# Optimization experiments

Hardware: AMD Instinct MI355X
Metric: run time of the kernel (lower is better)

## Reference

```python
import jax, jax.numpy as jnp
import numpy as np

WINDOW_SIZE = 128
NEG = -1e9

def setup_inputs() -> dict:
    key = jax.random.key(0)
    kq, kk, kv = jax.random.split(key, 3)
    B, H, T, D = 2, 16, 2048, 64
    q = jax.random.normal(kq, (B, H, T, D), dtype=jnp.float32)
    k = jax.random.normal(kk, (B, H, T, D), dtype=jnp.float32)
    v = jax.random.normal(kv, (B, H, T, D), dtype=jnp.float32)
    return {"q": q, "k": k, "v": v}

def reference(q, k, v):
    # q,k,v: (B, H, T, D)
    D = q.shape[-1]
    Tq, Tk = q.shape[2], k.shape[2]
    scale = 1.0 / jnp.sqrt(jnp.asarray(D, dtype=q.dtype))
    scores = jnp.einsum('bhqd,bhkd->bhqk', q, k) * scale  # (B,H,Tq,Tk)
    dist = jnp.abs(jnp.arange(Tq)[:, None] - jnp.arange(Tk)[None, :])
    window_mask = dist <= WINDOW_SIZE  # (Tq,Tk)
    scores = jnp.where(window_mask[None, None], scores, jnp.asarray(NEG, dtype=scores.dtype))
    attn = jax.nn.softmax(scores, axis=-1)
    output = jnp.einsum('bhqk,bhkd->bhqd', attn, v)
    return (output, attn)
```

## Files before the change

kernel.cpp:

```cpp
#include <hip/hip_runtime.h>
#include <hip/hip_bf16.h>

typedef short bf16x8 __attribute__((ext_vector_type(8)));
typedef short bf16x4 __attribute__((ext_vector_type(4)));
typedef float f32x4 __attribute__((ext_vector_type(4)));

#define T_DIM 2048
#define D_DIM 64
#define WIN 128
#define QBLK 64
#define ACCT 17
#define NEGBIG -1e30f

__device__ __forceinline__ short f2b(float x) {
  __hip_bfloat16 h = __float2bfloat16(x);
  return *reinterpret_cast<short*>(&h);
}
__device__ __forceinline__ float b2f(short s) {
  unsigned u = ((unsigned)(unsigned short)s) << 16;
  return __builtin_bit_cast(float, u);
}
__device__ __forceinline__ bf16x8 cvt8(f32x4 a, f32x4 b) {
  bf16x8 r;
  r[0] = f2b(a[0]); r[1] = f2b(a[1]); r[2] = f2b(a[2]); r[3] = f2b(a[3]);
  r[4] = f2b(b[0]); r[5] = f2b(b[1]); r[6] = f2b(b[2]); r[7] = f2b(b[3]);
  return r;
}
__device__ __forceinline__ int swz(int row, int b) { return row * 640 + (b ^ ((row & 7) << 4)); }

__global__ __launch_bounds__(256, 2) void lsa_one(
    const float* __restrict__ Qg, const float* __restrict__ Kg,
    const float* __restrict__ Vg, float* __restrict__ Og,
    float* __restrict__ Ag) {
  const int tid = threadIdx.x;
  const int work = ((blockIdx.x & 7) << 7) + (blockIdx.x >> 3);
  const int bh = work >> 5;
  const int q0 = (work & 31) * QBLK;
  int kstart = q0 - WIN; if (kstart < 0) kstart = 0;
  int kend = q0 + QBLK + WIN; if (kend > T_DIM) kend = T_DIM;
  const int KW = kend - kstart;
  const int nkt = KW >> 4;

  const float* qptr = Qg + (size_t)bh * (T_DIM * D_DIM);
  const float* kptr = Kg + (size_t)bh * (T_DIM * D_DIM);
  const float* vptr = Vg + (size_t)bh * (T_DIM * D_DIM);
  float* optr = Og + (size_t)bh * (T_DIM * D_DIM);
  float* aptr = Ag + (size_t)bh * ((size_t)T_DIM * T_DIM);

  __shared__ __align__(16) char Vb[D_DIM * 640];
  __shared__ __align__(16) char Pb[QBLK * 640];

  for (int idx = tid; idx < KW * 16; idx += 256) {
    const int r = idx >> 4, c4 = idx & 15;
    f32x4 f = *(const f32x4*)(vptr + (size_t)(kstart + r) * D_DIM + c4 * 4);
    const int d0 = c4 * 4;
    *(short*)(Vb + swz(d0 + 0, r * 2)) = f2b(f[0]);
    *(short*)(Vb + swz(d0 + 1, r * 2)) = f2b(f[1]);
    *(short*)(Vb + swz(d0 + 2, r * 2)) = f2b(f[2]);
    *(short*)(Vb + swz(d0 + 3, r * 2)) = f2b(f[3]);
  }

  const int lane = tid & 63, w = tid >> 6, c = lane & 15, hi = lane >> 4;

  const float* qrow = qptr + (size_t)(q0 + w * 16 + c) * D_DIM + 8 * hi;
  const bf16x8 qb0 = cvt8(*(const f32x4*)qrow, *(const f32x4*)(qrow + 4));
  const bf16x8 qb1 = cvt8(*(const f32x4*)(qrow + 32), *(const f32x4*)(qrow + 36));

  int klo = q0 + w * 16 - WIN - kstart; if (klo < 0) klo = 0;
  const int kt0 = klo >> 4;
  int kt1 = (q0 + w * 16 + 15 + WIN + 1 - kstart + 15) >> 4; if (kt1 > nkt) kt1 = nkt;
  const int s0 = kt0 >> 1, s1 = (kt1 + 1) >> 1;
  const int nlive = kt1 - kt0;

  f32x4 acc[ACCT];
#pragma unroll
  for (int i = 0; i < ACCT; ++i) {
    acc[i] = (f32x4){0.f, 0.f, 0.f, 0.f};
    if (i < nlive) {
      const float* kr = kptr + (size_t)(kstart + (kt0 + i) * 16 + c) * D_DIM + 8 * hi;
      const bf16x8 b0 = cvt8(*(const f32x4*)kr, *(const f32x4*)(kr + 4));
      const bf16x8 b1 = cvt8(*(const f32x4*)(kr + 32), *(const f32x4*)(kr + 36));
      acc[i] = __builtin_amdgcn_mfma_f32_16x16x32_bf16(b0, qb0, acc[i], 0, 0, 0);
      acc[i] = __builtin_amdgcn_mfma_f32_16x16x32_bf16(b1, qb1, acc[i], 0, 0, 0);
    }
  }

  const int qr = q0 + w * 16 + c;
  const int kb = kstart + 4 * hi;
  float m = NEGBIG;
#pragma unroll
  for (int i = 0; i < ACCT; ++i)
    if (i < nlive) {
#pragma unroll
      for (int j = 0; j < 4; ++j) {
        float s = acc[i][j] * 0.125f;
        const int kcol = kb + (kt0 + i) * 16 + j;
        int dist = qr - kcol; dist = dist < 0 ? -dist : dist;
        s = (dist <= WIN) ? s : NEGBIG;
        acc[i][j] = s;
        m = fmaxf(m, s);
      }
    }
  m = fmaxf(m, __shfl_xor(m, 16));
  m = fmaxf(m, __shfl_xor(m, 32));
  float sum = 0.f;
#pragma unroll
  for (int i = 0; i < ACCT; ++i)
    if (i < nlive) {
#pragma unroll
      for (int j = 0; j < 4; ++j) {
        const float p = __expf(acc[i][j] - m);
        acc[i][j] = p;
        sum += p;
      }
    }
  sum += __shfl_xor(sum, 16);
  sum += __shfl_xor(sum, 32);
  const float inv = 1.f / sum;

  const int prow = w * 16 + c;
#pragma unroll
  for (int i = 0; i < ACCT; ++i)
    if (i < nlive) {
      bf16x4 pk;
#pragma unroll
      for (int j = 0; j < 4; ++j) pk[j] = f2b(acc[i][j] * inv);
      *(bf16x4*)(Pb + swz(prow, 32 * (kt0 + i) + 8 * hi)) = pk;
    }
  {
    const bf16x4 z4 = {0, 0, 0, 0};
    for (int t = 0; t < kt0; ++t) *(bf16x4*)(Pb + swz(prow, 32 * t + 8 * hi)) = z4;
    for (int t = kt1; t < nkt; ++t) *(bf16x4*)(Pb + swz(prow, 32 * t + 8 * hi)) = z4;
  }

  for (int rr = 0; rr < 16; ++rr) {
    const int r = w * 16 + rr;
    float* dst = aptr + (size_t)(q0 + r) * T_DIM;
#pragma unroll
    for (int i = 0; i < 8; ++i) {
      const int col = i * 256 + lane * 4;
      f32x4 val = {0.f, 0.f, 0.f, 0.f};
      if (col >= kstart && col < kend) {
        const bf16x4 pv = *(const bf16x4*)(Pb + swz(r, (col - kstart) * 2));
        val[0] = b2f(pv[0]); val[1] = b2f(pv[1]); val[2] = b2f(pv[2]); val[3] = b2f(pv[3]);
      }
      __builtin_nontemporal_store(val, (f32x4*)(dst + col));
    }
  }

  __syncthreads();

  f32x4 ov[4];
#pragma unroll
  for (int dt = 0; dt < 4; ++dt) ov[dt] = (f32x4){0.f, 0.f, 0.f, 0.f};
  for (int s = s0; s < s1; ++s) {
    const bf16x8 pa = *(const bf16x8*)(Pb + swz(w * 16 + c, 64 * s + 16 * hi));
#pragma unroll
    for (int dt = 0; dt < 4; ++dt) {
      const bf16x8 vb = *(const bf16x8*)(Vb + swz(dt * 16 + c, 64 * s + 16 * hi));
      ov[dt] = __builtin_amdgcn_mfma_f32_16x16x32_bf16(pa, vb, ov[dt], 0, 0, 0);
    }
  }
#pragma unroll
  for (int dt = 0; dt < 4; ++dt)
#pragma unroll
    for (int j = 0; j < 4; ++j)
      __builtin_nontemporal_store(
          ov[dt][j], optr + (size_t)(q0 + w * 16 + 4 * hi + j) * D_DIM + dt * 16 + c);
}

extern "C" void kernel_launch(void* const* d_in, const int* in_sizes, int n_in,
                              void* d_out, int out_size, void* d_ws, size_t ws_size,
                              hipStream_t stream) {
  const float* q = (const float*)d_in[0];
  const float* k = (const float*)d_in[1];
  const float* v = (const float*)d_in[2];
  float* out = (float*)d_out;
  float* attn = out + (size_t)2 * 16 * T_DIM * D_DIM;
  lsa_one<<<dim3(2 * 16 * (T_DIM / QBLK)), dim3(256), 0, stream>>>(q, k, v, out, attn);
}
```

Before: 129.0 us.

## Pre-convert Q/K/V to bf16 in workspace and split into multi-kernel pipeline

Adds pre-pass kernels that convert Q and K to bf16 and write V transposed as bf16 into the workspace. The main kernel then reads bf16 operands directly, fetching V fragments from global memory instead of staging them in shared memory, which allows a third resident block per CU. It also writes the output tile before the attention-matrix stores. This removes the redundant per-block fp32-to-bf16 conversion of overlapping K and V windows, at the cost of three extra launches and an extra pass over the inputs. The original kernel remains as a fallback when the workspace is too small.

```diff
diff --git a/kernel.cpp b/kernel.cpp
--- a/kernel.cpp
+++ b/kernel.cpp
@@ -7,6 +7,8 @@
 
 #define T_DIM 2048
 #define D_DIM 64
+#define BH 32
+#define NELEM (BH * T_DIM * D_DIM)
 #define WIN 128
 #define QBLK 64
 #define ACCT 17
@@ -28,7 +30,171 @@
 }
 __device__ __forceinline__ int swz(int row, int b) { return row * 640 + (b ^ ((row & 7) << 4)); }
 
-__global__ __launch_bounds__(256, 2) void lsa_one(
+__global__ __launch_bounds__(256) void conv_qk(const float* __restrict__ A,
+                                               short* __restrict__ B) {
+  const size_t i = ((size_t)blockIdx.x * 256 + threadIdx.x) * 8;
+  const f32x4 a = *(const f32x4*)(A + i);
+  const f32x4 b = *(const f32x4*)(A + i + 4);
+  *(bf16x8*)(B + i) = cvt8(a, b);
+}
+
+__global__ __launch_bounds__(256) void conv_vt(const float* __restrict__ V,
+                                               short* __restrict__ Vt) {
+  __shared__ short Lt[64][65];
+  const int bh = blockIdx.x >> 5, k0 = (blockIdx.x & 31) * 64;
+  const int tid = threadIdx.x;
+  {
+    const int kr = tid >> 2, dq = tid & 3;
+    const float* src = V + ((size_t)(bh * T_DIM + k0 + kr)) * D_DIM + dq * 16;
+#pragma unroll
+    for (int g = 0; g < 4; ++g) {
+      const f32x4 f = *(const f32x4*)(src + g * 4);
+#pragma unroll
+      for (int j = 0; j < 4; ++j) Lt[kr][dq * 16 + g * 4 + j] = f2b(f[j]);
+    }
+  }
+  __syncthreads();
+  {
+    const int dr = tid >> 2, kc = tid & 3;
+    bf16x8 o0, o1;
+#pragma unroll
+    for (int j = 0; j < 8; ++j) {
+      o0[j] = Lt[kc * 16 + j][dr];
+      o1[j] = Lt[kc * 16 + 8 + j][dr];
+    }
+    short* dst = Vt + ((size_t)(bh * D_DIM + dr)) * T_DIM + k0 + kc * 16;
+    *(bf16x8*)dst = o0;
+    *(bf16x8*)(dst + 8) = o1;
+  }
+}
+
+__global__ __launch_bounds__(256, 3) void lsa_main(
+    const short* __restrict__ Q16, const short* __restrict__ K16,
+    const short* __restrict__ Vt16, float* __restrict__ Og, float* __restrict__ Ag) {
+  const int tid = threadIdx.x;
+  const int work = ((blockIdx.x & 7) << 7) + (blockIdx.x >> 3);
+  const int bh = work >> 5;
+  const int q0 = (work & 31) * QBLK;
+  int kstart = q0 - WIN; if (kstart < 0) kstart = 0;
+  int kend = q0 + QBLK + WIN; if (kend > T_DIM) kend = T_DIM;
+  const int nkt = (kend - kstart) >> 4;
+
+  float* optr = Og + (size_t)bh * (T_DIM * D_DIM);
+  float* aptr = Ag + (size_t)bh * ((size_t)T_DIM * T_DIM);
+
+  __shared__ __align__(16) char Pb[QBLK * 640];
+
+  const int lane = tid & 63, w = tid >> 6, c = lane & 15, hi = lane >> 4;
+
+  const short* qp = Q16 + ((size_t)(bh * T_DIM + q0 + w * 16 + c)) * D_DIM + 8 * hi;
+  const bf16x8 qb0 = *(const bf16x8*)qp;
+  const bf16x8 qb1 = *(const bf16x8*)(qp + 32);
+
+  int klo = q0 + w * 16 - WIN - kstart; if (klo < 0) klo = 0;
+  const int kt0 = klo >> 4;
+  int kt1 = (q0 + w * 16 + 15 + WIN + 1 - kstart + 15) >> 4; if (kt1 > nkt) kt1 = nkt;
+  const int s0 = kt0 >> 1, s1 = (kt1 + 1) >> 1;
+  const int nlive = kt1 - kt0;
+
+  f32x4 acc[ACCT];
+  const short* kbase = K16 + ((size_t)(bh * T_DIM + kstart + c)) * D_DIM + 8 * hi;
+#pragma unroll
+  for (int i = 0; i < ACCT; ++i) {
+    acc[i] = (f32x4){0.f, 0.f, 0.f, 0.f};
+    if (i < nlive) {
+      const short* kr = kbase + (size_t)((kt0 + i) * 16) * D_DIM;
+      const bf16x8 b0 = *(const bf16x8*)kr;
+      const bf16x8 b1 = *(const bf16x8*)(kr + 32);
+      acc[i] = __builtin_amdgcn_mfma_f32_16x16x32_bf16(b0, qb0, acc[i], 0, 0, 0);
+      acc[i] = __builtin_amdgcn_mfma_f32_16x16x32_bf16(b1, qb1, acc[i], 0, 0, 0);
+    }
+  }
+
+  const int qr = q0 + w * 16 + c;
+  const int kb = kstart + 4 * hi;
+  float m = NEGBIG;
+#pragma unroll
+  for (int i = 0; i < ACCT; ++i)
+    if (i < nlive) {
+#pragma unroll
+      for (int j = 0; j < 4; ++j) {
+        float s = acc[i][j] * 0.125f;
+        const int kcol = kb + (kt0 + i) * 16 + j;
+        int dist = qr - kcol; dist = dist < 0 ? -dist : dist;
+        s = (dist <= WIN) ? s : NEGBIG;
+        acc[i][j] = s;
+        m = fmaxf(m, s);
+      }
+    }
+  m = fmaxf(m, __shfl_xor(m, 16));
+  m = fmaxf(m, __shfl_xor(m, 32));
+  float sum = 0.f;
+#pragma unroll
+  for (int i = 0; i < ACCT; ++i)
+    if (i < nlive) {
+#pragma unroll
+      for (int j = 0; j < 4; ++j) {
+        const float p = __expf(acc[i][j] - m);
+        acc[i][j] = p;
+        sum += p;
+      }
+    }
+  sum += __shfl_xor(sum, 16);
+  sum += __shfl_xor(sum, 32);
+  const float inv = 1.f / sum;
+
+  const int prow = w * 16 + c;
+#pragma unroll
+  for (int i = 0; i < ACCT; ++i)
+    if (i < nlive) {
+      bf16x4 pk;
+#pragma unroll
+      for (int j = 0; j < 4; ++j) pk[j] = f2b(acc[i][j] * inv);
+      *(bf16x4*)(Pb + swz(prow, 32 * (kt0 + i) + 8 * hi)) = pk;
+    }
+  {
+    const bf16x4 z4 = {0, 0, 0, 0};
+    for (int t = 0; t < kt0; ++t) *(bf16x4*)(Pb + swz(prow, 32 * t + 8 * hi)) = z4;
+    for (int t = kt1; t < nkt; ++t) *(bf16x4*)(Pb + swz(prow, 32 * t + 8 * hi)) = z4;
+  }
+
+  f32x4 ov[4];
+#pragma unroll
+  for (int dt = 0; dt < 4; ++dt) ov[dt] = (f32x4){0.f, 0.f, 0.f, 0.f};
+  for (int s = s0; s < s1; ++s) {
+    const bf16x8 pa = *(const bf16x8*)(Pb + swz(w * 16 + c, 64 * s + 16 * hi));
+#pragma unroll
+    for (int dt = 0; dt < 4; ++dt) {
+      const short* vp = Vt16 + ((size_t)(bh * D_DIM + dt * 16 + c)) * T_DIM +
+                        kstart + 32 * s + 8 * hi;
+      const bf16x8 vb = *(const bf16x8*)vp;
+      ov[dt] = __builtin_amdgcn_mfma_f32_16x16x32_bf16(pa, vb, ov[dt], 0, 0, 0);
+    }
+  }
+#pragma unroll
+  for (int dt = 0; dt < 4; ++dt)
+#pragma unroll
+    for (int j = 0; j < 4; ++j)
+      __builtin_nontemporal_store(
+          ov[dt][j], optr + (size_t)(q0 + w * 16 + 4 * hi + j) * D_DIM + dt * 16 + c);
+
+  for (int rr = 0; rr < 16; ++rr) {
+    const int r = w * 16 + rr;
+    float* dst = aptr + (size_t)(q0 + r) * T_DIM;
+#pragma unroll
+    for (int i = 0; i < 8; ++i) {
+      const int col = i * 256 + lane * 4;
+      f32x4 val = {0.f, 0.f, 0.f, 0.f};
+      if (col >= kstart && col < kend) {
+        const bf16x4 pv = *(const bf16x4*)(Pb + swz(r, (col - kstart) * 2));
+        val[0] = b2f(pv[0]); val[1] = b2f(pv[1]); val[2] = b2f(pv[2]); val[3] = b2f(pv[3]);
+      }
+      __builtin_nontemporal_store(val, (f32x4*)(dst + col));
+    }
+  }
+}
+
+__global__ __launch_bounds__(256, 2) void lsa_fb(
     const float* __restrict__ Qg, const float* __restrict__ Kg,
     const float* __restrict__ Vg, float* __restrict__ Og,
     float* __restrict__ Ag) {
@@ -61,7 +227,6 @@
   }
 
   const int lane = tid & 63, w = tid >> 6, c = lane & 15, hi = lane >> 4;
-
   const float* qrow = qptr + (size_t)(q0 + w * 16 + c) * D_DIM + 8 * hi;
   const bf16x8 qb0 = cvt8(*(const f32x4*)qrow, *(const f32x4*)(qrow + 4));
   const bf16x8 qb1 = cvt8(*(const f32x4*)(qrow + 32), *(const f32x4*)(qrow + 36));
@@ -176,6 +341,18 @@
   const float* k = (const float*)d_in[1];
   const float* v = (const float*)d_in[2];
   float* out = (float*)d_out;
-  float* attn = out + (size_t)2 * 16 * T_DIM * D_DIM;
-  lsa_one<<<dim3(2 * 16 * (T_DIM / QBLK)), dim3(256), 0, stream>>>(q, k, v, out, attn);
-}
+  float* attn = out + (size_t)BH * T_DIM * D_DIM;
+
+  const size_t need = (size_t)3 * NELEM * sizeof(short);
+  if (ws_size >= need) {
+    short* q16 = (short*)d_ws;
+    short* k16 = q16 + NELEM;
+    short* vt16 = k16 + NELEM;
+    conv_qk<<<dim3(NELEM / 8 / 256), dim3(256), 0, stream>>>(q, q16);
+    conv_qk<<<dim3(NELEM / 8 / 256), dim3(256), 0, stream>>>(k, k16);
+    conv_vt<<<dim3(BH * (T_DIM / 64)), dim3(256), 0, stream>>>(v, vt16);
+    lsa_main<<<dim3(BH * (T_DIM / QBLK)), dim3(256), 0, stream>>>(q16, k16, vt16, out, attn);
+  } else {
+    lsa_fb<<<dim3(BH * (T_DIM / QBLK)), dim3(256), 0, stream>>>(q, k, v, out, attn);
+  }
+}
```

New measurement: 153.5 us. +19.0%, slower.

## Process two query blocks per workgroup and overlap attn-row stores with next block's compute

Applied to the files above, without the earlier changes.

Each workgroup now handles two adjacent 64-row query blocks in sequence. The large attention-matrix row sweep for the first block is deferred until after the second block's QK^T and softmax, so those global stores overlap with MFMA and exp work. The aim is to hide the store latency that dominates this output-bandwidth-bound kernel. In exchange the grid is halved, which reduces parallelism and keeps more live state in registers during the sweep.

```diff
diff --git a/kernel.cpp b/kernel.cpp
--- a/kernel.cpp
+++ b/kernel.cpp
@@ -28,28 +28,8 @@
 }
 __device__ __forceinline__ int swz(int row, int b) { return row * 640 + (b ^ ((row & 7) << 4)); }
 
-__global__ __launch_bounds__(256, 2) void lsa_one(
-    const float* __restrict__ Qg, const float* __restrict__ Kg,
-    const float* __restrict__ Vg, float* __restrict__ Og,
-    float* __restrict__ Ag) {
-  const int tid = threadIdx.x;
-  const int work = ((blockIdx.x & 7) << 7) + (blockIdx.x >> 3);
-  const int bh = work >> 5;
-  const int q0 = (work & 31) * QBLK;
-  int kstart = q0 - WIN; if (kstart < 0) kstart = 0;
-  int kend = q0 + QBLK + WIN; if (kend > T_DIM) kend = T_DIM;
-  const int KW = kend - kstart;
-  const int nkt = KW >> 4;
-
-  const float* qptr = Qg + (size_t)bh * (T_DIM * D_DIM);
-  const float* kptr = Kg + (size_t)bh * (T_DIM * D_DIM);
-  const float* vptr = Vg + (size_t)bh * (T_DIM * D_DIM);
-  float* optr = Og + (size_t)bh * (T_DIM * D_DIM);
-  float* aptr = Ag + (size_t)bh * ((size_t)T_DIM * T_DIM);
-
-  __shared__ __align__(16) char Vb[D_DIM * 640];
-  __shared__ __align__(16) char Pb[QBLK * 640];
-
+__device__ __forceinline__ void stage_v(const float* __restrict__ vptr, char* Vb,
+                                        int kstart, int KW, int tid) {
   for (int idx = tid; idx < KW * 16; idx += 256) {
     const int r = idx >> 4, c4 = idx & 15;
     f32x4 f = *(const f32x4*)(vptr + (size_t)(kstart + r) * D_DIM + c4 * 4);
@@ -59,9 +39,11 @@
     *(short*)(Vb + swz(d0 + 2, r * 2)) = f2b(f[2]);
     *(short*)(Vb + swz(d0 + 3, r * 2)) = f2b(f[3]);
   }
-
-  const int lane = tid & 63, w = tid >> 6, c = lane & 15, hi = lane >> 4;
-
+}
+
+__device__ __forceinline__ void compute_smax_p(
+    const float* __restrict__ qptr, const float* __restrict__ kptr, char* Pb,
+    int q0, int kstart, int nkt, int w, int c, int hi, int& kt0o, int& kt1o) {
   const float* qrow = qptr + (size_t)(q0 + w * 16 + c) * D_DIM + 8 * hi;
   const bf16x8 qb0 = cvt8(*(const f32x4*)qrow, *(const f32x4*)(qrow + 4));
   const bf16x8 qb1 = cvt8(*(const f32x4*)(qrow + 32), *(const f32x4*)(qrow + 36));
@@ -69,7 +51,6 @@
   int klo = q0 + w * 16 - WIN - kstart; if (klo < 0) klo = 0;
   const int kt0 = klo >> 4;
   int kt1 = (q0 + w * 16 + 15 + WIN + 1 - kstart + 15) >> 4; if (kt1 > nkt) kt1 = nkt;
-  const int s0 = kt0 >> 1, s1 = (kt1 + 1) >> 1;
   const int nlive = kt1 - kt0;
 
   f32x4 acc[ACCT];
@@ -132,7 +113,34 @@
     for (int t = 0; t < kt0; ++t) *(bf16x4*)(Pb + swz(prow, 32 * t + 8 * hi)) = z4;
     for (int t = kt1; t < nkt; ++t) *(bf16x4*)(Pb + swz(prow, 32 * t + 8 * hi)) = z4;
   }
-
+  kt0o = kt0; kt1o = kt1;
+}
+
+__device__ __forceinline__ void pv_store(const char* Pb, const char* Vb,
+                                         float* __restrict__ optr, int q0,
+                                         int kt0, int kt1, int w, int c, int hi) {
+  const int s0 = kt0 >> 1, s1 = (kt1 + 1) >> 1;
+  f32x4 ov[4];
+#pragma unroll
+  for (int dt = 0; dt < 4; ++dt) ov[dt] = (f32x4){0.f, 0.f, 0.f, 0.f};
+  for (int s = s0; s < s1; ++s) {
+    const bf16x8 pa = *(const bf16x8*)(Pb + swz(w * 16 + c, 64 * s + 16 * hi));
+#pragma unroll
+    for (int dt = 0; dt < 4; ++dt) {
+      const bf16x8 vb = *(const bf16x8*)(Vb + swz(dt * 16 + c, 64 * s + 16 * hi));
+      ov[dt] = __builtin_amdgcn_mfma_f32_16x16x32_bf16(pa, vb, ov[dt], 0, 0, 0);
+    }
+  }
+#pragma unroll
+  for (int dt = 0; dt < 4; ++dt)
+#pragma unroll
+    for (int j = 0; j < 4; ++j)
+      __builtin_nontemporal_store(
+          ov[dt][j], optr + (size_t)(q0 + w * 16 + 4 * hi + j) * D_DIM + dt * 16 + c);
+}
+
+__device__ __forceinline__ void sweep_rows(float* __restrict__ aptr, const char* Pb,
+                                           int q0, int kstart, int kend, int w, int lane) {
   for (int rr = 0; rr < 16; ++rr) {
     const int r = w * 16 + rr;
     float* dst = aptr + (size_t)(q0 + r) * T_DIM;
@@ -147,26 +155,119 @@
       __builtin_nontemporal_store(val, (f32x4*)(dst + col));
     }
   }
-
+}
+
+__global__ __launch_bounds__(256, 2) void lsa_pair(
+    const float* __restrict__ Qg, const float* __restrict__ Kg,
+    const float* __restrict__ Vg, float* __restrict__ Og,
+    float* __restrict__ Ag) {
+  const int tid = threadIdx.x;
+  const int pair = ((blockIdx.x & 7) << 6) + (blockIdx.x >> 3);
+  const int bh = pair >> 4;
+  const int q0A = (pair & 15) * (2 * QBLK);
+  const int q0B = q0A + QBLK;
+
+  const float* qptr = Qg + (size_t)bh * (T_DIM * D_DIM);
+  const float* kptr = Kg + (size_t)bh * (T_DIM * D_DIM);
+  const float* vptr = Vg + (size_t)bh * (T_DIM * D_DIM);
+  float* optr = Og + (size_t)bh * (T_DIM * D_DIM);
+  float* aptr = Ag + (size_t)bh * ((size_t)T_DIM * T_DIM);
+
+  __shared__ __align__(16) char Vb[D_DIM * 640];
+  __shared__ __align__(16) char Pb[QBLK * 640];
+
+  const int lane = tid & 63, w = tid >> 6, c = lane & 15, hi = lane >> 4;
+
+  int kstartA = q0A - WIN; if (kstartA < 0) kstartA = 0;
+  int kendA = q0A + QBLK + WIN; if (kendA > T_DIM) kendA = T_DIM;
+  const int nktA = (kendA - kstartA) >> 4;
+  int kstartB = q0B - WIN; if (kstartB < 0) kstartB = 0;
+  int kendB = q0B + QBLK + WIN; if (kendB > T_DIM) kendB = T_DIM;
+  const int nktB = (kendB - kstartB) >> 4;
+
+  stage_v(vptr, Vb, kstartA, kendA - kstartA, tid);
+  int kt0A, kt1A;
+  compute_smax_p(qptr, kptr, Pb, q0A, kstartA, nktA, w, c, hi, kt0A, kt1A);
   __syncthreads();
-
-  f32x4 ov[4];
-#pragma unroll
-  for (int dt = 0; dt < 4; ++dt) ov[dt] = (f32x4){0.f, 0.f, 0.f, 0.f};
-  for (int s = s0; s < s1; ++s) {
-    const bf16x8 pa = *(const bf16x8*)(Pb + swz(w * 16 + c, 64 * s + 16 * hi));
-#pragma unroll
-    for (int dt = 0; dt < 4; ++dt) {
-      const bf16x8 vb = *(const bf16x8*)(Vb + swz(dt * 16 + c, 64 * s + 16 * hi));
-      ov[dt] = __builtin_amdgcn_mfma_f32_16x16x32_bf16(pa, vb, ov[dt], 0, 0, 0);
-    }
-  }
-#pragma unroll
-  for (int dt = 0; dt < 4; ++dt)
-#pragma unroll
-    for (int j = 0; j < 4; ++j)
-      __builtin_nontemporal_store(
-          ov[dt][j], optr + (size_t)(q0 + w * 16 + 4 * hi + j) * D_DIM + dt * 16 + c);
+  pv_store(Pb, Vb, optr, q0A, kt0A, kt1A, w, c, hi);
+  __syncthreads();
+
+  stage_v(vptr, Vb, kstartB, kendB - kstartB, tid);
+  int kt0B, kt1B;
+  {
+    const float* qrow = qptr + (size_t)(q0B + w * 16 + c) * D_DIM + 8 * hi;
+    const bf16x8 qb0 = cvt8(*(const f32x4*)qrow, *(const f32x4*)(qrow + 4));
+    const bf16x8 qb1 = cvt8(*(const f32x4*)(qrow + 32), *(const f32x4*)(qrow + 36));
+    int klo = q0B + w * 16 - WIN - kstartB; if (klo < 0) klo = 0;
+    const int kt0 = klo >> 4;
+    int kt1 = (q0B + w * 16 + 15 + WIN + 1 - kstartB + 15) >> 4; if (kt1 > nktB) kt1 = nktB;
+    const int nlive = kt1 - kt0;
+    f32x4 acc[ACCT];
+#pragma unroll
+    for (int i = 0; i < ACCT; ++i) {
+      acc[i] = (f32x4){0.f, 0.f, 0.f, 0.f};
+      if (i < nlive) {
+        const float* kr = kptr + (size_t)(kstartB + (kt0 + i) * 16 + c) * D_DIM + 8 * hi;
+        const bf16x8 b0 = cvt8(*(const f32x4*)kr, *(const f32x4*)(kr + 4));
+        const bf16x8 b1 = cvt8(*(const f32x4*)(kr + 32), *(const f32x4*)(kr + 36));
+        acc[i] = __builtin_amdgcn_mfma_f32_16x16x32_bf16(b0, qb0, acc[i], 0, 0, 0);
+        acc[i] = __builtin_amdgcn_mfma_f32_16x16x32_bf16(b1, qb1, acc[i], 0, 0, 0);
+      }
+    }
+    const int qr = q0B + w * 16 + c;
+    const int kb = kstartB + 4 * hi;
+    float m = NEGBIG;
+#pragma unroll
+    for (int i = 0; i < ACCT; ++i)
+      if (i < nlive) {
+#pragma unroll
+        for (int j = 0; j < 4; ++j) {
+          float s = acc[i][j] * 0.125f;
+          const int kcol = kb + (kt0 + i) * 16 + j;
+          int dist = qr - kcol; dist = dist < 0 ? -dist : dist;
+          s = (dist <= WIN) ? s : NEGBIG;
+          acc[i][j] = s;
+          m = fmaxf(m, s);
+        }
+      }
+    m = fmaxf(m, __shfl_xor(m, 16));
+    m = fmaxf(m, __shfl_xor(m, 32));
+    float sum = 0.f;
+#pragma unroll
+    for (int i = 0; i < ACCT; ++i)
+      if (i < nlive) {
+#pragma unroll
+        for (int j = 0; j < 4; ++j) {
+          const float p = __expf(acc[i][j] - m);
+          acc[i][j] = p;
+          sum += p;
+        }
+      }
+    sum += __shfl_xor(sum, 16);
+    sum += __shfl_xor(sum, 32);
+    const float inv = 1.f / sum;
+
+    sweep_rows(aptr, Pb, q0A, kstartA, kendA, w, lane);
+
+    const int prow = w * 16 + c;
+#pragma unroll
+    for (int i = 0; i < ACCT; ++i)
+      if (i < nlive) {
+        bf16x4 pk;
+#pragma unroll
+        for (int j = 0; j < 4; ++j) pk[j] = f2b(acc[i][j] * inv);
+        *(bf16x4*)(Pb + swz(prow, 32 * (kt0 + i) + 8 * hi)) = pk;
+      }
+    {
+      const bf16x4 z4 = {0, 0, 0, 0};
+      for (int t = 0; t < kt0; ++t) *(bf16x4*)(Pb + swz(prow, 32 * t + 8 * hi)) = z4;
+      for (int t = kt1; t < nktB; ++t) *(bf16x4*)(Pb + swz(prow, 32 * t + 8 * hi)) = z4;
+    }
+    kt0B = kt0; kt1B = kt1;
+  }
+  __syncthreads();
+  pv_store(Pb, Vb, optr, q0B, kt0B, kt1B, w, c, hi);
+  sweep_rows(aptr, Pb, q0B, kstartB, kendB, w, lane);
 }
 
 extern "C" void kernel_launch(void* const* d_in, const int* in_sizes, int n_in,
@@ -177,5 +278,5 @@
   const float* v = (const float*)d_in[2];
   float* out = (float*)d_out;
   float* attn = out + (size_t)2 * 16 * T_DIM * D_DIM;
-  lsa_one<<<dim3(2 * 16 * (T_DIM / QBLK)), dim3(256), 0, stream>>>(q, k, v, out, attn);
-}
+  lsa_pair<<<dim3(2 * 16 * (T_DIM / (2 * QBLK))), dim3(256), 0, stream>>>(q, k, v, out, attn);
+}
```

Measured after the change: 147.1 us. +14.0%, slower.
